# Kernel tuning notes

Hardware: AMD Instinct MI355X
Metric: run time of the kernel (lower is better)

## Reference

```python
import jax, jax.numpy as jnp
import numpy as np

HEADS = 4
DIM_HEAD = 32
EPS = 1e-5


def setup_inputs() -> dict:
    key = jax.random.key(0)
    ks = jax.random.split(key, 3)
    B, H, W, C = 16, 64, 64, 128
    hidden = HEADS * DIM_HEAD  # 128
    x = jax.random.normal(ks[0], (B, H, W, C), dtype=jnp.float32)
    w_qkv = jax.random.normal(ks[1], (C, 3 * hidden), dtype=jnp.float32) * 0.05
    w_out = jax.random.normal(ks[2], (hidden, C), dtype=jnp.float32) * 0.05
    b_out = jnp.zeros((C,), dtype=jnp.float32)
    g_ln = jnp.ones((C,), dtype=jnp.float32)
    b_ln = jnp.zeros((C,), dtype=jnp.float32)
    return {"x": x, "w_qkv": w_qkv, "w_out": w_out, "b_out": b_out,
            "g_ln": g_ln, "b_ln": b_ln}


def reference(x, w_qkv, w_out, b_out, g_ln, b_ln):
    B, H, W, C = x.shape
    scale = DIM_HEAD ** -0.5
    n = H * W
    # 1x1 conv == channel matmul: [B,H,W,C] @ [C,3*hidden]
    qkv = jnp.einsum('bhwc,cf->bhwf', x, w_qkv)
    q, k, v = jnp.split(qkv, 3, axis=-1)
    # rearrange 'b x y (h c) -> b h c (x y)'
    def to_heads(t):
        return t.reshape(B, n, HEADS, DIM_HEAD).transpose(0, 2, 3, 1)  # [B,h,d,n]
    q, k, v = map(to_heads, (q, k, v))
    q = jax.nn.softmax(q, axis=-2) * scale   # softmax over channel dim d
    k = jax.nn.softmax(k, axis=-1)           # softmax over spatial dim n
    context = jnp.einsum('bhdn,bhen->bhde', k, v)  # [B,h,d,e] small
    out = jnp.einsum('bhde,bhdn->bhen', context, q)  # [B,h,e,n]
    # rearrange 'b h c (x y) -> b x y (h c)'
    out = out.transpose(0, 3, 1, 2).reshape(B, H, W, HEADS * DIM_HEAD)
    # to_out: 1x1 conv with bias, then LayerNorm over last dim
    out = jnp.einsum('bhwc,cd->bhwd', out, w_out) + b_out
    mean = jnp.mean(out, axis=-1, keepdims=True)
    var = jnp.var(out, axis=-1, keepdims=True)
    out = (out - mean) / jnp.sqrt(var + EPS) * g_ln + b_ln
    return out
```

## Files before the change

### kernel.cpp

```cpp
#include <hip/hip_runtime.h>
#include <hip/hip_bf16.h>
#include <cstddef>
#include <cstdint>


typedef __attribute__((ext_vector_type(8))) short short8_t;
typedef __attribute__((ext_vector_type(4))) short short4_t;
typedef __attribute__((ext_vector_type(4))) float f32x4;

#define SCALE_Q 0.17677669529663687f
#define EPS_LN 1e-5f

__device__ __forceinline__ unsigned short f2bf(float f) {
  union { float f; unsigned u; } v; v.f = f;
  unsigned r = (v.u + 0x7FFFu + ((v.u >> 16) & 1u)) >> 16;
  return (unsigned short)r;
}
__device__ __forceinline__ float bf2f(unsigned short u) {
  union { float f; unsigned u; } v; v.u = ((unsigned)u) << 16;
  return v.f;
}

__device__ __forceinline__ short8_t trunc8(float4 lo, float4 hi) {
  union { float4 f; unsigned u[4]; } a, b;
  union { unsigned u[4]; short8_t s; } r;
  a.f = lo; b.f = hi;
  r.u[0] = __builtin_amdgcn_perm(a.u[1], a.u[0], 0x07060302);
  r.u[1] = __builtin_amdgcn_perm(a.u[3], a.u[2], 0x07060302);
  r.u[2] = __builtin_amdgcn_perm(b.u[1], b.u[0], 0x07060302);
  r.u[3] = __builtin_amdgcn_perm(b.u[3], b.u[2], 0x07060302);
  return r.s;
}

__global__ void k_transpose_wqkv(const float* __restrict__ w,
                                 unsigned short* __restrict__ wT) {
  int idx = blockIdx.x * 256 + threadIdx.x;
  int k = idx / 384;
  int c = idx - k * 384;
  wT[c * 128 + k] = f2bf(w[idx]);
}

__global__ __launch_bounds__(256, 2)
void k_kv_ctx(const float* __restrict__ x, const unsigned short* __restrict__ wT,
              float* __restrict__ ctxp, float* __restrict__ ksump) {
  __shared__ short Bk[128][136];
  __shared__ short Bv[128][136];

  int tid = threadIdx.x;
  int rb = blockIdx.x;
  int rowBase = rb * 128;

  {
    const unsigned short* wk = wT + (size_t)1 * 128 * 128;
    const unsigned short* wv2 = wT + (size_t)2 * 128 * 128;
#pragma unroll
    for (int i = 0; i < 8; ++i) {
      int idx = i * 256 + tid;
      int n = idx >> 4;
      int k8 = (idx & 15) << 3;
      *(short8_t*)&Bk[n][k8] = *(const short8_t*)(wk + (size_t)n * 128 + k8);
      *(short8_t*)&Bv[n][k8] = *(const short8_t*)(wv2 + (size_t)n * 128 + k8);
    }
  }

  int lane = tid & 63;
  int wv = tid >> 6;
  int wr = wv >> 1, wc = wv & 1;
  int lr = lane & 15;
  int kg = lane >> 4;

  short8_t abf[4][4];
  {
    const float* ap = x + (size_t)(rowBase + wr * 64 + lr) * 128 + kg * 8;
#pragma unroll
    for (int mf = 0; mf < 4; ++mf) {
      const float* r = ap + (size_t)mf * 16 * 128;
#pragma unroll
      for (int kk = 0; kk < 4; ++kk)
        abf[kk][mf] = trunc8(*(const float4*)(r + kk * 32),
                             *(const float4*)(r + kk * 32 + 4));
    }
  }
  __syncthreads();

  uint2 ekp[4][4], vp[4][4];
  {
    f32x4 acc[4][4] = {};
#pragma unroll
    for (int kk = 0; kk < 4; ++kk) {
      short8_t bf[4];
#pragma unroll
      for (int nf = 0; nf < 4; ++nf)
        bf[nf] = *(const short8_t*)&Bk[wc * 64 + nf * 16 + lr][kk * 32 + kg * 8];
#pragma unroll
      for (int mf = 0; mf < 4; ++mf)
#pragma unroll
        for (int nf = 0; nf < 4; ++nf)
          acc[mf][nf] = __builtin_amdgcn_mfma_f32_16x16x32_bf16(abf[kk][mf], bf[nf], acc[mf][nf], 0, 0, 0);
    }
#pragma unroll
    for (int mf = 0; mf < 4; ++mf)
#pragma unroll
      for (int nf = 0; nf < 4; ++nf) {
        unsigned s0 = f2bf(__expf(acc[mf][nf][0])), s1 = f2bf(__expf(acc[mf][nf][1]));
        unsigned s2 = f2bf(__expf(acc[mf][nf][2])), s3 = f2bf(__expf(acc[mf][nf][3]));
        ekp[mf][nf].x = s0 | (s1 << 16);
        ekp[mf][nf].y = s2 | (s3 << 16);
      }
  }
  {
    f32x4 acc[4][4] = {};
#pragma unroll
    for (int kk = 0; kk < 4; ++kk) {
      short8_t bf[4];
#pragma unroll
      for (int nf = 0; nf < 4; ++nf)
        bf[nf] = *(const short8_t*)&Bv[wc * 64 + nf * 16 + lr][kk * 32 + kg * 8];
#pragma unroll
      for (int mf = 0; mf < 4; ++mf)
#pragma unroll
        for (int nf = 0; nf < 4; ++nf)
          acc[mf][nf] = __builtin_amdgcn_mfma_f32_16x16x32_bf16(abf[kk][mf], bf[nf], acc[mf][nf], 0, 0, 0);
    }
#pragma unroll
    for (int mf = 0; mf < 4; ++mf)
#pragma unroll
      for (int nf = 0; nf < 4; ++nf) {
        unsigned s0 = f2bf(acc[mf][nf][0]), s1 = f2bf(acc[mf][nf][1]);
        unsigned s2 = f2bf(acc[mf][nf][2]), s3 = f2bf(acc[mf][nf][3]);
        vp[mf][nf].x = s0 | (s1 << 16);
        vp[mf][nf].y = s2 | (s3 << 16);
      }
  }
  __syncthreads();

  short (*ekT)[136] = Bk;
  short (*vT)[136] = Bv;
#pragma unroll
  for (int mf = 0; mf < 4; ++mf) {
    int t0 = wr * 64 + mf * 16 + kg * 4;
#pragma unroll
    for (int nf = 0; nf < 4; ++nf) {
      int col = wc * 64 + nf * 16 + lr;
      *(uint2*)&ekT[col][t0] = ekp[mf][nf];
      *(uint2*)&vT[col][t0] = vp[mf][nf];
    }
  }
  __syncthreads();

  {
    int h = wv;
    f32x4 c2[2][2] = {};
#pragma unroll
    for (int kk = 0; kk < 4; ++kk) {
      short8_t a2[2], b2[2];
#pragma unroll
      for (int m2 = 0; m2 < 2; ++m2)
        a2[m2] = *(const short8_t*)&ekT[h * 32 + m2 * 16 + lr][kk * 32 + kg * 8];
#pragma unroll
      for (int n2 = 0; n2 < 2; ++n2)
        b2[n2] = *(const short8_t*)&vT[h * 32 + n2 * 16 + lr][kk * 32 + kg * 8];
#pragma unroll
      for (int m2 = 0; m2 < 2; ++m2)
#pragma unroll
        for (int n2 = 0; n2 < 2; ++n2)
          c2[m2][n2] = __builtin_amdgcn_mfma_f32_16x16x32_bf16(a2[m2], b2[n2], c2[m2][n2], 0, 0, 0);
    }
    float* cp = ctxp + ((size_t)rb * 4 + h) * 1024;
#pragma unroll
    for (int m2 = 0; m2 < 2; ++m2)
#pragma unroll
      for (int n2 = 0; n2 < 2; ++n2)
#pragma unroll
        for (int j = 0; j < 4; ++j) {
          int d = m2 * 16 + kg * 4 + j;
          int e = n2 * 16 + lr;
          cp[d * 32 + e] = c2[m2][n2][j];
        }
  }

  if (tid < 128) {
    float s = 0;
#pragma unroll
    for (int t8 = 0; t8 < 128; t8 += 8) {
      short8_t v8 = *(const short8_t*)&ekT[tid][t8];
#pragma unroll
      for (int i = 0; i < 8; ++i) s += bf2f((unsigned short)v8[i]);
    }
    ksump[(size_t)rb * 128 + tid] = s;
  }
}

__global__ __launch_bounds__(256, 1)
void k_weff(const float* __restrict__ ctxp, const float* __restrict__ ksump,
            const float* __restrict__ wout, unsigned short* __restrict__ weffT) {
  __shared__ float wo[128][128];
  __shared__ float ctxn[4][32][32];
  __shared__ float ks[4][32];
  int tid = threadIdx.x;
  int b = blockIdx.x;
#pragma unroll
  for (int i = 0; i < 64; ++i) {
    int idx = i * 256 + tid;
    ((float*)wo)[idx] = wout[idx];
  }
  if (tid < 128) {
    int h = tid >> 5, d = tid & 31;
    float s = 0;
    for (int c = 0; c < 32; ++c)
      s += ksump[((size_t)(b * 32 + c)) * 128 + tid];
    ks[h][d] = s;
  }
  __syncthreads();
  for (int i = 0; i < 16; ++i) {
    int idx = i * 256 + tid;
    int h = idx >> 10, d = (idx >> 5) & 31;
    float s = 0;
    for (int c = 0; c < 32; ++c)
      s += ctxp[(((size_t)(b * 32 + c) * 4 + h) << 10) + (idx & 1023)];
    ctxn[h][d][idx & 31] = s / ks[h][d];
  }
  __syncthreads();
  int hd = tid & 127;
  int h = hd >> 5, d = hd & 31;
  int jBase = (tid >> 7) * 64;
  float cx[32];
#pragma unroll
  for (int e = 0; e < 32; ++e) cx[e] = ctxn[h][d][e];
  unsigned short* outp = weffT + (size_t)b * 16384;
  for (int jj = 0; jj < 64; ++jj) {
    int j = jBase + jj;
    float s = 0;
#pragma unroll
    for (int e = 0; e < 32; ++e) s += cx[e] * wo[h * 32 + e][j];
    outp[(size_t)j * 128 + hd] = f2bf(s);
  }
}

__global__ __launch_bounds__(256, 2)
void k_qout_ln(const float* __restrict__ x, const unsigned short* __restrict__ wT,
               const unsigned short* __restrict__ weffT,
               const float* __restrict__ b_out, const float* __restrict__ g_ln,
               const float* __restrict__ b_ln, float* __restrict__ out) {
  __shared__ short Bs[128][136];
  __shared__ short Qs[128][136];
  __shared__ float2 red[128][2];

  int tid = threadIdx.x;
  int rowBase = blockIdx.x * 128;
  int b = rowBase >> 12;

  {
#pragma unroll
    for (int i = 0; i < 8; ++i) {
      int idx = i * 256 + tid;
      int n = idx >> 4;
      int k8 = (idx & 15) << 3;
      *(short8_t*)&Bs[n][k8] = *(const short8_t*)(wT + (size_t)n * 128 + k8);
    }
  }

  short8_t b2reg[8];
  {
    const unsigned short* bb = weffT + (size_t)b * 16384;
#pragma unroll
    for (int i = 0; i < 8; ++i) {
      int idx = i * 256 + tid;
      int n = idx >> 4;
      int k8 = (idx & 15) << 3;
      b2reg[i] = *(const short8_t*)(bb + (size_t)n * 128 + k8);
    }
  }

  int lane = tid & 63;
  int wv = tid >> 6;
  int wr = wv >> 1, wc = wv & 1;
  int lr = lane & 15;
  int kg = lane >> 4;

  short8_t abf[4][4];
  {
    const float* ap = x + (size_t)(rowBase + wr * 64 + lr) * 128 + kg * 8;
#pragma unroll
    for (int mf = 0; mf < 4; ++mf) {
      const float* r = ap + (size_t)mf * 16 * 128;
#pragma unroll
      for (int kk = 0; kk < 4; ++kk)
        abf[kk][mf] = trunc8(*(const float4*)(r + kk * 32),
                             *(const float4*)(r + kk * 32 + 4));
    }
  }
  __syncthreads();

  f32x4 acc[4][4] = {};
#pragma unroll
  for (int kk = 0; kk < 4; ++kk) {
    short8_t bf[4];
#pragma unroll
    for (int nf = 0; nf < 4; ++nf)
      bf[nf] = *(const short8_t*)&Bs[wc * 64 + nf * 16 + lr][kk * 32 + kg * 8];
#pragma unroll
    for (int mf = 0; mf < 4; ++mf)
#pragma unroll
      for (int nf = 0; nf < 4; ++nf)
        acc[mf][nf] = __builtin_amdgcn_mfma_f32_16x16x32_bf16(abf[kk][mf], bf[nf], acc[mf][nf], 0, 0, 0);
  }

#pragma unroll
  for (int hg = 0; hg < 2; ++hg) {
#pragma unroll
    for (int mf = 0; mf < 4; ++mf) {
#pragma unroll
      for (int j = 0; j < 4; ++j) {
        float v0 = acc[mf][hg * 2][j], v1 = acc[mf][hg * 2 + 1][j];
        float m = fmaxf(v0, v1);
#pragma unroll
        for (int d = 1; d < 16; d <<= 1) m = fmaxf(m, __shfl_xor(m, d, 64));
        float e0 = __expf(v0 - m), e1 = __expf(v1 - m);
        float s = e0 + e1;
#pragma unroll
        for (int d = 1; d < 16; d <<= 1) s += __shfl_xor(s, d, 64);
        float inv = SCALE_Q / s;
        int r = wr * 64 + mf * 16 + kg * 4 + j;
        int c0 = wc * 64 + hg * 32 + lr;
        Qs[r][c0] = (short)f2bf(e0 * inv);
        Qs[r][c0 + 16] = (short)f2bf(e1 * inv);
      }
    }
  }
  __syncthreads();

  {
#pragma unroll
    for (int i = 0; i < 8; ++i) {
      int idx = i * 256 + tid;
      int n = idx >> 4;
      int k8 = (idx & 15) << 3;
      *(short8_t*)&Bs[n][k8] = b2reg[i];
    }
  }
  __syncthreads();

  f32x4 acc2[4][4] = {};
#pragma unroll
  for (int kk = 0; kk < 4; ++kk) {
    short8_t a2[4], bf[4];
#pragma unroll
    for (int mf = 0; mf < 4; ++mf)
      a2[mf] = *(const short8_t*)&Qs[wr * 64 + mf * 16 + lr][kk * 32 + kg * 8];
#pragma unroll
    for (int nf = 0; nf < 4; ++nf)
      bf[nf] = *(const short8_t*)&Bs[wc * 64 + nf * 16 + lr][kk * 32 + kg * 8];
#pragma unroll
    for (int mf = 0; mf < 4; ++mf)
#pragma unroll
      for (int nf = 0; nf < 4; ++nf)
        acc2[mf][nf] = __builtin_amdgcn_mfma_f32_16x16x32_bf16(a2[mf], bf[nf], acc2[mf][nf], 0, 0, 0);
  }

  int colc[4]; float bo[4], gl[4], bl[4];
#pragma unroll
  for (int nf = 0; nf < 4; ++nf) {
    int c = wc * 64 + nf * 16 + lr;
    colc[nf] = c; bo[nf] = b_out[c]; gl[nf] = g_ln[c]; bl[nf] = b_ln[c];
  }
#pragma unroll
  for (int mf = 0; mf < 4; ++mf)
#pragma unroll
    for (int nf = 0; nf < 4; ++nf)
#pragma unroll
      for (int j = 0; j < 4; ++j) acc2[mf][nf][j] += bo[nf];

#pragma unroll
  for (int mf = 0; mf < 4; ++mf) {
    float s[4] = {0, 0, 0, 0}, q[4] = {0, 0, 0, 0};
#pragma unroll
    for (int nf = 0; nf < 4; ++nf)
#pragma unroll
      for (int j = 0; j < 4; ++j) {
        float v = acc2[mf][nf][j];
        s[j] += v; q[j] += v * v;
      }
#pragma unroll
    for (int j = 0; j < 4; ++j) {
#pragma unroll
      for (int d = 1; d < 16; d <<= 1) {
        s[j] += __shfl_xor(s[j], d, 64);
        q[j] += __shfl_xor(q[j], d, 64);
      }
    }
    if (lr == 0) {
#pragma unroll
      for (int j = 0; j < 4; ++j)
        red[wr * 64 + mf * 16 + kg * 4 + j][wc] = make_float2(s[j], q[j]);
    }
  }
  __syncthreads();
#pragma unroll
  for (int mf = 0; mf < 4; ++mf) {
#pragma unroll
    for (int j = 0; j < 4; ++j) {
      int rloc = wr * 64 + mf * 16 + kg * 4 + j;
      float2 r0 = red[rloc][0], r1 = red[rloc][1];
      float mean = (r0.x + r1.x) * (1.0f / 128.0f);
      float var = (r0.y + r1.y) * (1.0f / 128.0f) - mean * mean;
      float rstd = rsqrtf(var + EPS_LN);
      size_t ro = (size_t)(rowBase + rloc) * 128;
#pragma unroll
      for (int nf = 0; nf < 4; ++nf)
        out[ro + colc[nf]] = (acc2[mf][nf][j] - mean) * rstd * gl[nf] + bl[nf];
    }
  }
}

extern "C" void kernel_launch(void* const* d_in, const int* in_sizes, int n_in,
                              void* d_out, int out_size, void* d_ws, size_t ws_size,
                              hipStream_t stream) {
  const float* x     = (const float*)d_in[0];
  const float* w_qkv = (const float*)d_in[1];
  const float* w_out = (const float*)d_in[2];
  const float* b_out = (const float*)d_in[3];
  const float* g_ln  = (const float*)d_in[4];
  const float* b_ln  = (const float*)d_in[5];
  float* out = (float*)d_out;

  char* ws = (char*)d_ws;
  unsigned short* wqkvT = (unsigned short*)(ws + 0);
  float* ctxp           = (float*)(ws + 131072);
  float* ksump          = (float*)(ws + 131072 + 8388608);
  unsigned short* weffT = (unsigned short*)(ws + 131072 + 8388608 + 262144);

  k_transpose_wqkv<<<192, 256, 0, stream>>>(w_qkv, wqkvT);
  k_kv_ctx<<<512, 256, 0, stream>>>(x, wqkvT, ctxp, ksump);
  k_weff<<<16, 256, 0, stream>>>(ctxp, ksump, w_out, weffT);
  k_qout_ln<<<512, 256, 0, stream>>>(x, wqkvT, weffT, b_out, g_ln, b_ln, out);
}
```

Before: 69.64 us.

## Compute Q projection and softmax in first pass, store bf16 Q for output kernel

Moves the Q projection and its channel softmax into the K/V context kernel, so x is read only once and Q is written to the workspace as bf16. The output kernel now loads the precomputed Q and does only the projection with the effective weights plus LayerNorm, with each wave covering full rows so no shared-memory reduction or block barriers are needed. B-operand weights are read directly from global memory instead of being staged in LDS. The weff kernel is split per head across 64 blocks to raise parallelism. The Q softmax drops its max subtraction, which risks overflow for large logits, and the extra Q write and read add global traffic.

```diff
diff --git a/kernel.cpp b/kernel.cpp
--- a/kernel.cpp
+++ b/kernel.cpp
@@ -5,7 +5,6 @@
 
 
 typedef __attribute__((ext_vector_type(8))) short short8_t;
-typedef __attribute__((ext_vector_type(4))) short short4_t;
 typedef __attribute__((ext_vector_type(4))) float f32x4;
 
 #define SCALE_Q 0.17677669529663687f
@@ -41,27 +40,15 @@
 }
 
 __global__ __launch_bounds__(256, 2)
-void k_kv_ctx(const float* __restrict__ x, const unsigned short* __restrict__ wT,
-              float* __restrict__ ctxp, float* __restrict__ ksump) {
-  __shared__ short Bk[128][136];
-  __shared__ short Bv[128][136];
+void k_qkv_ctx(const float* __restrict__ x, const unsigned short* __restrict__ wT,
+               float* __restrict__ ctxp, float* __restrict__ ksump,
+               unsigned short* __restrict__ qs) {
+  __shared__ short ekT[128][136];
+  __shared__ short vT[128][136];
 
   int tid = threadIdx.x;
   int rb = blockIdx.x;
   int rowBase = rb * 128;
-
-  {
-    const unsigned short* wk = wT + (size_t)1 * 128 * 128;
-    const unsigned short* wv2 = wT + (size_t)2 * 128 * 128;
-#pragma unroll
-    for (int i = 0; i < 8; ++i) {
-      int idx = i * 256 + tid;
-      int n = idx >> 4;
-      int k8 = (idx & 15) << 3;
-      *(short8_t*)&Bk[n][k8] = *(const short8_t*)(wk + (size_t)n * 128 + k8);
-      *(short8_t*)&Bv[n][k8] = *(const short8_t*)(wv2 + (size_t)n * 128 + k8);
-    }
-  }
 
   int lane = tid & 63;
   int wv = tid >> 6;
@@ -81,9 +68,14 @@
                              *(const float4*)(r + kk * 32 + 4));
     }
   }
-  __syncthreads();
-
-  uint2 ekp[4][4], vp[4][4];
+
+  const unsigned short* wq = wT;
+  const unsigned short* wk = wT + 16384;
+  const unsigned short* wvv = wT + 32768;
+  int bRow[4];
+#pragma unroll
+  for (int nf = 0; nf < 4; ++nf) bRow[nf] = (wc * 64 + nf * 16 + lr) * 128;
+
   {
     f32x4 acc[4][4] = {};
 #pragma unroll
@@ -91,7 +83,7 @@
       short8_t bf[4];
 #pragma unroll
       for (int nf = 0; nf < 4; ++nf)
-        bf[nf] = *(const short8_t*)&Bk[wc * 64 + nf * 16 + lr][kk * 32 + kg * 8];
+        bf[nf] = *(const short8_t*)(wk + bRow[nf] + kk * 32 + kg * 8);
 #pragma unroll
       for (int mf = 0; mf < 4; ++mf)
 #pragma unroll
@@ -99,14 +91,16 @@
           acc[mf][nf] = __builtin_amdgcn_mfma_f32_16x16x32_bf16(abf[kk][mf], bf[nf], acc[mf][nf], 0, 0, 0);
     }
 #pragma unroll
-    for (int mf = 0; mf < 4; ++mf)
+    for (int mf = 0; mf < 4; ++mf) {
+      int t0 = wr * 64 + mf * 16 + kg * 4;
 #pragma unroll
       for (int nf = 0; nf < 4; ++nf) {
         unsigned s0 = f2bf(__expf(acc[mf][nf][0])), s1 = f2bf(__expf(acc[mf][nf][1]));
         unsigned s2 = f2bf(__expf(acc[mf][nf][2])), s3 = f2bf(__expf(acc[mf][nf][3]));
-        ekp[mf][nf].x = s0 | (s1 << 16);
-        ekp[mf][nf].y = s2 | (s3 << 16);
-      }
+        uint2 p; p.x = s0 | (s1 << 16); p.y = s2 | (s3 << 16);
+        *(uint2*)&ekT[wc * 64 + nf * 16 + lr][t0] = p;
+      }
+    }
   }
   {
     f32x4 acc[4][4] = {};
@@ -115,7 +109,7 @@
       short8_t bf[4];
 #pragma unroll
       for (int nf = 0; nf < 4; ++nf)
-        bf[nf] = *(const short8_t*)&Bv[wc * 64 + nf * 16 + lr][kk * 32 + kg * 8];
+        bf[nf] = *(const short8_t*)(wvv + bRow[nf] + kk * 32 + kg * 8);
 #pragma unroll
       for (int mf = 0; mf < 4; ++mf)
 #pragma unroll
@@ -123,29 +117,32 @@
           acc[mf][nf] = __builtin_amdgcn_mfma_f32_16x16x32_bf16(abf[kk][mf], bf[nf], acc[mf][nf], 0, 0, 0);
     }
 #pragma unroll
-    for (int mf = 0; mf < 4; ++mf)
+    for (int mf = 0; mf < 4; ++mf) {
+      int t0 = wr * 64 + mf * 16 + kg * 4;
 #pragma unroll
       for (int nf = 0; nf < 4; ++nf) {
         unsigned s0 = f2bf(acc[mf][nf][0]), s1 = f2bf(acc[mf][nf][1]);
         unsigned s2 = f2bf(acc[mf][nf][2]), s3 = f2bf(acc[mf][nf][3]);
-        vp[mf][nf].x = s0 | (s1 << 16);
-        vp[mf][nf].y = s2 | (s3 << 16);
-      }
-  }
-  __syncthreads();
-
-  short (*ekT)[136] = Bk;
-  short (*vT)[136] = Bv;
-#pragma unroll
-  for (int mf = 0; mf < 4; ++mf) {
-    int t0 = wr * 64 + mf * 16 + kg * 4;
-#pragma unroll
-    for (int nf = 0; nf < 4; ++nf) {
-      int col = wc * 64 + nf * 16 + lr;
-      *(uint2*)&ekT[col][t0] = ekp[mf][nf];
-      *(uint2*)&vT[col][t0] = vp[mf][nf];
-    }
-  }
+        uint2 p; p.x = s0 | (s1 << 16); p.y = s2 | (s3 << 16);
+        *(uint2*)&vT[wc * 64 + nf * 16 + lr][t0] = p;
+      }
+    }
+  }
+
+  f32x4 qacc[4][4] = {};
+#pragma unroll
+  for (int kk = 0; kk < 4; ++kk) {
+    short8_t bf[4];
+#pragma unroll
+    for (int nf = 0; nf < 4; ++nf)
+      bf[nf] = *(const short8_t*)(wq + bRow[nf] + kk * 32 + kg * 8);
+#pragma unroll
+    for (int mf = 0; mf < 4; ++mf)
+#pragma unroll
+      for (int nf = 0; nf < 4; ++nf)
+        qacc[mf][nf] = __builtin_amdgcn_mfma_f32_16x16x32_bf16(abf[kk][mf], bf[nf], qacc[mf][nf], 0, 0, 0);
+  }
+
   __syncthreads();
 
   {
@@ -172,11 +169,8 @@
 #pragma unroll
       for (int n2 = 0; n2 < 2; ++n2)
 #pragma unroll
-        for (int j = 0; j < 4; ++j) {
-          int d = m2 * 16 + kg * 4 + j;
-          int e = n2 * 16 + lr;
-          cp[d * 32 + e] = c2[m2][n2][j];
-        }
+        for (int j = 0; j < 4; ++j)
+          cp[(m2 * 16 + kg * 4 + j) * 32 + n2 * 16 + lr] = c2[m2][n2][j];
   }
 
   if (tid < 128) {
@@ -189,196 +183,135 @@
     }
     ksump[(size_t)rb * 128 + tid] = s;
   }
-}
-
-__global__ __launch_bounds__(256, 1)
-void k_weff(const float* __restrict__ ctxp, const float* __restrict__ ksump,
-            const float* __restrict__ wout, unsigned short* __restrict__ weffT) {
-  __shared__ float wo[128][128];
-  __shared__ float ctxn[4][32][32];
-  __shared__ float ks[4][32];
+
+#pragma unroll
+  for (int hg = 0; hg < 2; ++hg) {
+#pragma unroll
+    for (int mf = 0; mf < 4; ++mf) {
+#pragma unroll
+      for (int j = 0; j < 4; ++j) {
+        float e0 = __expf(qacc[mf][hg * 2][j]);
+        float e1 = __expf(qacc[mf][hg * 2 + 1][j]);
+        float s = e0 + e1;
+#pragma unroll
+        for (int d = 1; d < 16; d <<= 1) s += __shfl_xor(s, d, 64);
+        float inv = SCALE_Q / s;
+        int tok = rowBase + wr * 64 + mf * 16 + kg * 4 + j;
+        int hd = wc * 64 + hg * 32 + lr;
+        qs[(size_t)tok * 128 + hd] = f2bf(e0 * inv);
+        qs[(size_t)tok * 128 + hd + 16] = f2bf(e1 * inv);
+      }
+    }
+  }
+}
+
+__global__ __launch_bounds__(256, 4)
+void k_weff64(const float* __restrict__ ctxp, const float* __restrict__ ksump,
+              const float* __restrict__ wout, unsigned short* __restrict__ weffT) {
+  __shared__ float wo[32][128];
+  __shared__ float cn[32][32];
+  __shared__ float ksh[32];
   int tid = threadIdx.x;
-  int b = blockIdx.x;
-#pragma unroll
-  for (int i = 0; i < 64; ++i) {
+  int b = blockIdx.x >> 2, h = blockIdx.x & 3;
+
+#pragma unroll
+  for (int i = 0; i < 16; ++i) {
     int idx = i * 256 + tid;
-    ((float*)wo)[idx] = wout[idx];
-  }
-  if (tid < 128) {
-    int h = tid >> 5, d = tid & 31;
+    int e = idx >> 7, jj = idx & 127;
+    wo[e][jj] = wout[(h * 32 + e) * 128 + jj];
+  }
+  if (tid < 32) {
     float s = 0;
     for (int c = 0; c < 32; ++c)
-      s += ksump[((size_t)(b * 32 + c)) * 128 + tid];
-    ks[h][d] = s;
+      s += ksump[(size_t)(b * 32 + c) * 128 + h * 32 + tid];
+    ksh[tid] = s;
   }
   __syncthreads();
-  for (int i = 0; i < 16; ++i) {
+#pragma unroll
+  for (int i = 0; i < 4; ++i) {
     int idx = i * 256 + tid;
-    int h = idx >> 10, d = (idx >> 5) & 31;
+    int d = idx >> 5, e = idx & 31;
     float s = 0;
     for (int c = 0; c < 32; ++c)
-      s += ctxp[(((size_t)(b * 32 + c) * 4 + h) << 10) + (idx & 1023)];
-    ctxn[h][d][idx & 31] = s / ks[h][d];
+      s += ctxp[((size_t)(b * 32 + c) * 4 + h) * 1024 + idx];
+    cn[d][e] = s / ksh[d];
   }
   __syncthreads();
-  int hd = tid & 127;
-  int h = hd >> 5, d = hd & 31;
-  int jBase = (tid >> 7) * 64;
-  float cx[32];
-#pragma unroll
-  for (int e = 0; e < 32; ++e) cx[e] = ctxn[h][d][e];
-  unsigned short* outp = weffT + (size_t)b * 16384;
-  for (int jj = 0; jj < 64; ++jj) {
-    int j = jBase + jj;
+
+  int j = tid >> 1, dg = tid & 1;
+  unsigned short acc16[16];
+#pragma unroll
+  for (int dd = 0; dd < 16; ++dd) {
+    int d = dg * 16 + dd;
     float s = 0;
 #pragma unroll
-    for (int e = 0; e < 32; ++e) s += cx[e] * wo[h * 32 + e][j];
-    outp[(size_t)j * 128 + hd] = f2bf(s);
-  }
+    for (int e = 0; e < 32; ++e) s += cn[d][e] * wo[e][j];
+    acc16[dd] = f2bf(s);
+  }
+  unsigned short* outp = weffT + (size_t)b * 16384 + j * 128 + h * 32 + dg * 16;
+  *(short8_t*)outp = *(short8_t*)&acc16[0];
+  *(short8_t*)(outp + 8) = *(short8_t*)&acc16[8];
 }
 
 __global__ __launch_bounds__(256, 2)
-void k_qout_ln(const float* __restrict__ x, const unsigned short* __restrict__ wT,
-               const unsigned short* __restrict__ weffT,
-               const float* __restrict__ b_out, const float* __restrict__ g_ln,
-               const float* __restrict__ b_ln, float* __restrict__ out) {
-  __shared__ short Bs[128][136];
-  __shared__ short Qs[128][136];
-  __shared__ float2 red[128][2];
-
+void k_out_ln(const unsigned short* __restrict__ qs, const unsigned short* __restrict__ weffT,
+              const float* __restrict__ b_out, const float* __restrict__ g_ln,
+              const float* __restrict__ b_ln, float* __restrict__ out) {
   int tid = threadIdx.x;
   int rowBase = blockIdx.x * 128;
   int b = rowBase >> 12;
-
-  {
-#pragma unroll
-    for (int i = 0; i < 8; ++i) {
-      int idx = i * 256 + tid;
-      int n = idx >> 4;
-      int k8 = (idx & 15) << 3;
-      *(short8_t*)&Bs[n][k8] = *(const short8_t*)(wT + (size_t)n * 128 + k8);
-    }
-  }
-
-  short8_t b2reg[8];
-  {
-    const unsigned short* bb = weffT + (size_t)b * 16384;
-#pragma unroll
-    for (int i = 0; i < 8; ++i) {
-      int idx = i * 256 + tid;
-      int n = idx >> 4;
-      int k8 = (idx & 15) << 3;
-      b2reg[i] = *(const short8_t*)(bb + (size_t)n * 128 + k8);
-    }
-  }
-
   int lane = tid & 63;
-  int wv = tid >> 6;
-  int wr = wv >> 1, wc = wv & 1;
+  int w = tid >> 6;
   int lr = lane & 15;
   int kg = lane >> 4;
 
-  short8_t abf[4][4];
-  {
-    const float* ap = x + (size_t)(rowBase + wr * 64 + lr) * 128 + kg * 8;
-#pragma unroll
-    for (int mf = 0; mf < 4; ++mf) {
-      const float* r = ap + (size_t)mf * 16 * 128;
+  const unsigned short* bb = weffT + (size_t)b * 16384;
+
+  short8_t a[2][4];
+  {
+    const unsigned short* ap = qs + (size_t)(rowBase + w * 32 + lr) * 128 + kg * 8;
+#pragma unroll
+    for (int mf = 0; mf < 2; ++mf)
 #pragma unroll
       for (int kk = 0; kk < 4; ++kk)
-        abf[kk][mf] = trunc8(*(const float4*)(r + kk * 32),
-                             *(const float4*)(r + kk * 32 + 4));
-    }
-  }
-  __syncthreads();
-
-  f32x4 acc[4][4] = {};
+        a[mf][kk] = *(const short8_t*)(ap + (size_t)mf * 16 * 128 + kk * 32);
+  }
+
+  f32x4 acc[2][8] = {};
 #pragma unroll
   for (int kk = 0; kk < 4; ++kk) {
-    short8_t bf[4];
-#pragma unroll
-    for (int nf = 0; nf < 4; ++nf)
-      bf[nf] = *(const short8_t*)&Bs[wc * 64 + nf * 16 + lr][kk * 32 + kg * 8];
-#pragma unroll
-    for (int mf = 0; mf < 4; ++mf)
-#pragma unroll
-      for (int nf = 0; nf < 4; ++nf)
-        acc[mf][nf] = __builtin_amdgcn_mfma_f32_16x16x32_bf16(abf[kk][mf], bf[nf], acc[mf][nf], 0, 0, 0);
-  }
-
-#pragma unroll
-  for (int hg = 0; hg < 2; ++hg) {
-#pragma unroll
-    for (int mf = 0; mf < 4; ++mf) {
+    short8_t bf[8];
+#pragma unroll
+    for (int nf = 0; nf < 8; ++nf)
+      bf[nf] = *(const short8_t*)(bb + (size_t)(nf * 16 + lr) * 128 + kk * 32 + kg * 8);
+#pragma unroll
+    for (int mf = 0; mf < 2; ++mf)
+#pragma unroll
+      for (int nf = 0; nf < 8; ++nf)
+        acc[mf][nf] = __builtin_amdgcn_mfma_f32_16x16x32_bf16(a[mf][kk], bf[nf], acc[mf][nf], 0, 0, 0);
+  }
+
+  float bo[8], gl[8], bl[8];
+#pragma unroll
+  for (int nf = 0; nf < 8; ++nf) {
+    int c = nf * 16 + lr;
+    bo[nf] = b_out[c]; gl[nf] = g_ln[c]; bl[nf] = b_ln[c];
+  }
+#pragma unroll
+  for (int mf = 0; mf < 2; ++mf)
+#pragma unroll
+    for (int nf = 0; nf < 8; ++nf)
+#pragma unroll
+      for (int j = 0; j < 4; ++j) acc[mf][nf][j] += bo[nf];
+
+#pragma unroll
+  for (int mf = 0; mf < 2; ++mf) {
+    float s[4] = {0, 0, 0, 0}, q[4] = {0, 0, 0, 0};
+#pragma unroll
+    for (int nf = 0; nf < 8; ++nf)
 #pragma unroll
       for (int j = 0; j < 4; ++j) {
-        float v0 = acc[mf][hg * 2][j], v1 = acc[mf][hg * 2 + 1][j];
-        float m = fmaxf(v0, v1);
-#pragma unroll
-        for (int d = 1; d < 16; d <<= 1) m = fmaxf(m, __shfl_xor(m, d, 64));
-        float e0 = __expf(v0 - m), e1 = __expf(v1 - m);
-        float s = e0 + e1;
-#pragma unroll
-        for (int d = 1; d < 16; d <<= 1) s += __shfl_xor(s, d, 64);
-        float inv = SCALE_Q / s;
-        int r = wr * 64 + mf * 16 + kg * 4 + j;
-        int c0 = wc * 64 + hg * 32 + lr;
-        Qs[r][c0] = (short)f2bf(e0 * inv);
-        Qs[r][c0 + 16] = (short)f2bf(e1 * inv);
-      }
-    }
-  }
-  __syncthreads();
-
-  {
-#pragma unroll
-    for (int i = 0; i < 8; ++i) {
-      int idx = i * 256 + tid;
-      int n = idx >> 4;
-      int k8 = (idx & 15) << 3;
-      *(short8_t*)&Bs[n][k8] = b2reg[i];
-    }
-  }
-  __syncthreads();
-
-  f32x4 acc2[4][4] = {};
-#pragma unroll
-  for (int kk = 0; kk < 4; ++kk) {
-    short8_t a2[4], bf[4];
-#pragma unroll
-    for (int mf = 0; mf < 4; ++mf)
-      a2[mf] = *(const short8_t*)&Qs[wr * 64 + mf * 16 + lr][kk * 32 + kg * 8];
-#pragma unroll
-    for (int nf = 0; nf < 4; ++nf)
-      bf[nf] = *(const short8_t*)&Bs[wc * 64 + nf * 16 + lr][kk * 32 + kg * 8];
-#pragma unroll
-    for (int mf = 0; mf < 4; ++mf)
-#pragma unroll
-      for (int nf = 0; nf < 4; ++nf)
-        acc2[mf][nf] = __builtin_amdgcn_mfma_f32_16x16x32_bf16(a2[mf], bf[nf], acc2[mf][nf], 0, 0, 0);
-  }
-
-  int colc[4]; float bo[4], gl[4], bl[4];
-#pragma unroll
-  for (int nf = 0; nf < 4; ++nf) {
-    int c = wc * 64 + nf * 16 + lr;
-    colc[nf] = c; bo[nf] = b_out[c]; gl[nf] = g_ln[c]; bl[nf] = b_ln[c];
-  }
-#pragma unroll
-  for (int mf = 0; mf < 4; ++mf)
-#pragma unroll
-    for (int nf = 0; nf < 4; ++nf)
-#pragma unroll
-      for (int j = 0; j < 4; ++j) acc2[mf][nf][j] += bo[nf];
-
-#pragma unroll
-  for (int mf = 0; mf < 4; ++mf) {
-    float s[4] = {0, 0, 0, 0}, q[4] = {0, 0, 0, 0};
-#pragma unroll
-    for (int nf = 0; nf < 4; ++nf)
-#pragma unroll
-      for (int j = 0; j < 4; ++j) {
-        float v = acc2[mf][nf][j];
+        float v = acc[mf][nf][j];
         s[j] += v; q[j] += v * v;
       }
 #pragma unroll
@@ -389,26 +322,15 @@
         q[j] += __shfl_xor(q[j], d, 64);
       }
     }
-    if (lr == 0) {
-#pragma unroll
-      for (int j = 0; j < 4; ++j)
-        red[wr * 64 + mf * 16 + kg * 4 + j][wc] = make_float2(s[j], q[j]);
-    }
-  }
-  __syncthreads();
-#pragma unroll
-  for (int mf = 0; mf < 4; ++mf) {
 #pragma unroll
     for (int j = 0; j < 4; ++j) {
-      int rloc = wr * 64 + mf * 16 + kg * 4 + j;
-      float2 r0 = red[rloc][0], r1 = red[rloc][1];
-      float mean = (r0.x + r1.x) * (1.0f / 128.0f);
-      float var = (r0.y + r1.y) * (1.0f / 128.0f) - mean * mean;
+      float mean = s[j] * (1.0f / 128.0f);
+      float var = q[j] * (1.0f / 128.0f) - mean * mean;
       float rstd = rsqrtf(var + EPS_LN);
-      size_t ro = (size_t)(rowBase + rloc) * 128;
-#pragma unroll
-      for (int nf = 0; nf < 4; ++nf)
-        out[ro + colc[nf]] = (acc2[mf][nf][j] - mean) * rstd * gl[nf] + bl[nf];
+      size_t ro = (size_t)(rowBase + w * 32 + mf * 16 + kg * 4 + j) * 128;
+#pragma unroll
+      for (int nf = 0; nf < 8; ++nf)
+        out[ro + nf * 16 + lr] = (acc[mf][nf][j] - mean) * rstd * gl[nf] + bl[nf];
     }
   }
 }
@@ -429,9 +351,10 @@
   float* ctxp           = (float*)(ws + 131072);
   float* ksump          = (float*)(ws + 131072 + 8388608);
   unsigned short* weffT = (unsigned short*)(ws + 131072 + 8388608 + 262144);
+  unsigned short* qs    = (unsigned short*)(ws + 131072 + 8388608 + 262144 + 524288);
 
   k_transpose_wqkv<<<192, 256, 0, stream>>>(w_qkv, wqkvT);
-  k_kv_ctx<<<512, 256, 0, stream>>>(x, wqkvT, ctxp, ksump);
-  k_weff<<<16, 256, 0, stream>>>(ctxp, ksump, w_out, weffT);
-  k_qout_ln<<<512, 256, 0, stream>>>(x, wqkvT, weffT, b_out, g_ln, b_ln, out);
-}
+  k_qkv_ctx<<<512, 256, 0, stream>>>(x, wqkvT, ctxp, ksump, qs);
+  k_weff64<<<64, 256, 0, stream>>>(ctxp, ksump, w_out, weffT);
+  k_out_ln<<<512, 256, 0, stream>>>(qs, weffT, b_out, g_ln, b_ln, out);
+}
```

Result: faster. 62.16 us (-10.7%).
